# Optimization experiments

Hardware: AMD Instinct MI355X
Metric: run time of the kernel (lower is better)

Reference implementation:

```python
import jax, jax.numpy as jnp
import numpy as np
from jax import lax

B, N, D, H, K = 8, 1024, 384, 6, 7
HD = D // H
EPS = 1e-5


def layer_norm(x, g, b):
    m = jnp.mean(x, axis=-1, keepdims=True)
    v = jnp.mean(jnp.square(x - m), axis=-1, keepdims=True)
    return (x - m) * lax.rsqrt(v + EPS) * g + b


def setup_inputs() -> dict:
    key = jax.random.key(0)
    ks = jax.random.split(key, 12)
    s = 0.02
    return {
        "x": jax.random.normal(ks[0], (B, N, D), jnp.float32),
        "qkv_w": jax.random.normal(ks[1], (3 * D, D), jnp.float32) * s,
        "qkv_b": jnp.zeros((3 * D,), jnp.float32),
        "proj_w": jax.random.normal(ks[2], (D, D), jnp.float32) * s,
        "proj_b": jnp.zeros((D,), jnp.float32),
        "t_before": jnp.eye(H, dtype=jnp.float32) + jax.random.normal(ks[3], (H, H), jnp.float32) * 0.01,
        "t_after": jnp.eye(H, dtype=jnp.float32) + jax.random.normal(ks[4], (H, H), jnp.float32) * 0.01,
        "dw_w": jax.random.normal(ks[5], (D, 1, K), jnp.float32) * s,
        "dw_b": jnp.zeros((D,), jnp.float32),
        "mlp_ln_g": jnp.ones((D,), jnp.float32),
        "mlp_ln_b": jnp.zeros((D,), jnp.float32),
        "norm1_g": jnp.ones((D,), jnp.float32),
        "norm1_b": jnp.zeros((D,), jnp.float32),
        "norm2_g": jnp.ones((D,), jnp.float32),
        "norm2_b": jnp.zeros((D,), jnp.float32),
        "fc1_w": jax.random.normal(ks[6], (4 * D, D), jnp.float32) * s,
        "fc1_b": jnp.zeros((4 * D,), jnp.float32),
        "fc2_w": jax.random.normal(ks[7], (D, 4 * D), jnp.float32) * s,
        "fc2_b": jnp.zeros((D,), jnp.float32),
    }


def reference(x, qkv_w, qkv_b, proj_w, proj_b, t_before, t_after, dw_w, dw_b,
              mlp_ln_g, mlp_ln_b, norm1_g, norm1_b, norm2_g, norm2_b,
              fc1_w, fc1_b, fc2_w, fc2_b):
    # ---- attention branch ----
    h = layer_norm(x, norm1_g, norm1_b)
    qkv = h @ qkv_w.T + qkv_b                                  # (B,N,3D)
    qkv = qkv.reshape(B, N, 3, H, HD).transpose(2, 0, 3, 1, 4)  # (3,B,H,N,hd)
    q, k, v = qkv[0], qkv[1], qkv[2]
    scale = HD ** -0.5
    scores = jnp.einsum('bhnd,bhmd->bhnm', q, k) * scale        # (B,H,N,N)
    scores = jnp.einsum('gh,bhnm->bgnm', t_before, scores)       # head-mix pre-softmax
    probs = jax.nn.softmax(scores, axis=-1)
    probs = jnp.einsum('gh,bhnm->bgnm', t_after, probs)          # head-mix post-softmax
    attn_out = jnp.einsum('bhnm,bhmd->bhnd', probs, v)           # (B,H,N,hd)
    attn_out = attn_out.transpose(0, 2, 1, 3).reshape(B, N, D)
    attn_out = attn_out @ proj_w.T + proj_b
    x = x + attn_out
    # ---- MLP branch ----
    h = layer_norm(x, norm2_g, norm2_b)
    # depthwise conv1d over tokens: (B,D,N), groups=D, same padding
    h_t = h.transpose(0, 2, 1)
    h_t = lax.conv_general_dilated(h_t, dw_w, window_strides=(1,),
                                   padding=[(K // 2, K // 2)],
                                   dimension_numbers=('NCH', 'OIH', 'NCH'),
                                   feature_group_count=D)
    h = h_t.transpose(0, 2, 1) + dw_b
    h = layer_norm(h, mlp_ln_g, mlp_ln_b)
    h = jax.nn.gelu(h @ fc1_w.T + fc1_b, approximate=False)
    h = h @ fc2_w.T + fc2_b
    return x + h
```

## Files before the change

kernel.cpp:

```cpp
#include <hip/hip_runtime.h>
#include <hip/hip_bf16.h>

#define BB 8
#define NN 1024
#define DD 384
#define HH 6
#define HD 64
#define BN 8192
#define D3 1152
#define D4 1536
#define SEC 3145728

typedef __attribute__((ext_vector_type(8))) short short8;
typedef __attribute__((ext_vector_type(4))) float f32x4;

typedef __attribute__((address_space(3))) unsigned char as3_byte;
typedef __attribute__((address_space(1))) const unsigned char as1_byte;

__device__ __forceinline__ void gload16(const void* g, void* l){
  __builtin_amdgcn_global_load_lds((as1_byte*)g, (as3_byte*)l, 16, 0, 0);
}

__device__ __forceinline__ float b2f(unsigned short u){
  union{unsigned int i; float f;} x; x.i=((unsigned int)u)<<16; return x.f;
}
__device__ __forceinline__ unsigned short f2b(float f){
  unsigned int u=__float_as_uint(f);
  return (unsigned short)((u + 0x7FFFu + ((u>>16)&1u))>>16);
}

__global__ void cvt_kernel(const float* __restrict__ w0, const float* __restrict__ w1,
                           const float* __restrict__ w2, const float* __restrict__ w3,
                           unsigned short* __restrict__ out){
  int i = blockIdx.x*256 + threadIdx.x;
  float v;
  if (i < 442368)        v = w0[i];
  else if (i < 589824)   v = w1[i - 442368];
  else if (i < 1179648)  v = w2[i - 589824];
  else if (i < 1769472)  v = w3[i - 1179648];
  else return;
  out[i] = f2b(v);
}

template<int OUTBF>
__global__ __launch_bounds__(128)
void ln_kernel(const float* __restrict__ in, const float* __restrict__ gg, const float* __restrict__ bb,
               float* __restrict__ outf, unsigned short* __restrict__ outb){
  int row = blockIdx.x, t = threadIdx.x;
  const float* r = in + (size_t)row*DD;
  float v0=r[t], v1=r[t+128], v2=r[t+256];
  float s=v0+v1+v2, q=v0*v0+v1*v1+v2*v2;
  #pragma unroll
  for (int o=32;o>0;o>>=1){ s+=__shfl_down(s,o); q+=__shfl_down(q,o); }
  __shared__ float ls[2], lq[2];
  if ((t&63)==0){ ls[t>>6]=s; lq[t>>6]=q; }
  __syncthreads();
  float S=ls[0]+ls[1], Q=lq[0]+lq[1];
  float mean=S*(1.0f/DD);
  float rstd=rsqrtf(Q*(1.0f/DD)-mean*mean+1e-5f);
  float o0=(v0-mean)*rstd*gg[t]+bb[t];
  float o1=(v1-mean)*rstd*gg[t+128]+bb[t+128];
  float o2=(v2-mean)*rstd*gg[t+256]+bb[t+256];
  if (OUTBF){ unsigned short* o=outb+(size_t)row*DD; o[t]=f2b(o0); o[t+128]=f2b(o1); o[t+256]=f2b(o2); }
  else      { float* o=outf+(size_t)row*DD; o[t]=o0; o[t+128]=o1; o[t+256]=o2; }
}

__global__ __launch_bounds__(128)
void conv_ln_kernel(const float* __restrict__ h2, const float* __restrict__ dww, const float* __restrict__ dwb,
                    const float* __restrict__ gg, const float* __restrict__ bb, unsigned short* __restrict__ out){
  int row=blockIdx.x, t=threadIdx.x;
  int bi=row>>10, n=row&1023;
  const float* base = h2 + (size_t)(bi<<10)*DD;
  float a[3];
  #pragma unroll
  for (int j=0;j<3;j++){
    int d=t+j*128;
    float acc=dwb[d];
    #pragma unroll
    for (int k=0;k<7;k++){
      int nn=n+k-3;
      if (nn>=0 && nn<NN) acc += dww[d*7+k]*base[(size_t)nn*DD + d];
    }
    a[j]=acc;
  }
  float s=a[0]+a[1]+a[2], q=a[0]*a[0]+a[1]*a[1]+a[2]*a[2];
  #pragma unroll
  for (int o=32;o>0;o>>=1){ s+=__shfl_down(s,o); q+=__shfl_down(q,o); }
  __shared__ float ls[2], lq[2];
  if ((t&63)==0){ ls[t>>6]=s; lq[t>>6]=q; }
  __syncthreads();
  float S=ls[0]+ls[1], Q=lq[0]+lq[1];
  float mean=S*(1.0f/DD);
  float rstd=rsqrtf(Q*(1.0f/DD)-mean*mean+1e-5f);
  unsigned short* o = out + (size_t)row*DD;
  #pragma unroll
  for (int j=0;j<3;j++){
    int d=t+j*128;
    o[d]=f2b((a[j]-mean)*rstd*gg[d]+bb[d]);
  }
}

template<int MODE, int TN>
__global__ __launch_bounds__(256)
void gemm_kernel(const unsigned short* __restrict__ A, const unsigned short* __restrict__ W,
                 const float* __restrict__ bias, const float* __restrict__ resid,
                 float* __restrict__ outf, unsigned short* __restrict__ outb,
                 int Kdim, int Ncols){
  constexpr int JF = TN/32;
  __shared__ __align__(16) unsigned short lds_a[2][128*32];
  __shared__ __align__(16) unsigned short lds_b[2][TN*32];
  int t=threadIdx.x, lane=t&63, w=t>>6;
  int bm = blockIdx.x*128;
  int bn = blockIdx.y*TN;
  int wr = w>>1, wc = w&1;
  int rm = lane&15, r16 = lane>>4;
  f32x4 acc[4][JF] = {};
  char* ldsa_c = (char*)lds_a;
  char* ldsb_c = (char*)lds_b;
  int abyte[4], bbyte[JF];
  #pragma unroll
  for (int i=0;i<4;i++){
    int ra = wr*64 + i*16 + rm;
    abyte[i] = ra*64 + ((r16 ^ ((ra>>1)&3))*16);
  }
  #pragma unroll
  for (int j=0;j<JF;j++){
    int rb = wc*(TN/2) + j*16 + rm;
    bbyte[j] = rb*64 + ((r16 ^ ((rb>>1)&3))*16);
  }
  auto stage = [&](int buf, int k0){
    #pragma unroll
    for (int c=0;c<2;c++){
      int u = t + c*256;
      int row = u>>2, sl = (u&3) ^ ((row>>1)&3);
      gload16(A + (size_t)(bm+row)*Kdim + k0 + sl*8, ldsa_c + buf*8192 + u*16);
    }
    #pragma unroll
    for (int c=0;c<TN/64;c++){
      int u = t + c*256;
      int row = u>>2, sl = (u&3) ^ ((row>>1)&3);
      gload16(W + (size_t)(bn+row)*Kdim + k0 + sl*8, ldsb_c + buf*(TN*64) + u*16);
    }
  };
  int niter = Kdim>>5;
  stage(0, 0);
  __syncthreads();
  for (int it=0; it<niter; ++it){
    if (it+1<niter) stage((it+1)&1, (it+1)<<5);
    int ab = (it&1)*8192, bb2 = (it&1)*(TN*64);
    short8 af[4], bf[JF];
    #pragma unroll
    for (int i=0;i<4;i++) af[i]=*reinterpret_cast<const short8*>(ldsa_c + ab + abyte[i]);
    #pragma unroll
    for (int j=0;j<JF;j++) bf[j]=*reinterpret_cast<const short8*>(ldsb_c + bb2 + bbyte[j]);
    #pragma unroll
    for (int i=0;i<4;i++)
      #pragma unroll
      for (int j=0;j<JF;j++)
        acc[i][j]=__builtin_amdgcn_mfma_f32_16x16x32_bf16(af[i],bf[j],acc[i][j],0,0,0);
    __syncthreads();
  }
  #pragma unroll
  for (int i=0;i<4;i++){
    #pragma unroll
    for (int j=0;j<JF;j++){
      #pragma unroll
      for (int r=0;r<4;r++){
        int row = bm + wr*64 + i*16 + r16*4 + r;
        int col = bn + wc*(TN/2) + j*16 + rm;
        float v = acc[i][j][r] + bias[col];
        if (MODE==0){
          int c = col/384; int rem = col - c*384; int hh = rem>>6, d = rem&63;
          if (c==0) v *= 0.125f;
          int bi = row>>10, nn = row&1023;
          outb[(size_t)c*SEC + (((size_t)(bi*6+hh))<<16) + (nn<<6) + d] = f2b(v);
        } else if (MODE==1){
          size_t idx = (size_t)row*Ncols + col;
          outf[idx] = resid[idx] + v;
        } else {
          float ge = 0.5f*v*(1.0f+erff(v*0.70710678118654752f));
          outb[(size_t)row*Ncols + col] = f2b(ge);
        }
      }
    }
  }
}

__global__ __launch_bounds__(256)
void vt8_kernel(const unsigned short* __restrict__ V, unsigned char* __restrict__ V8){
  __shared__ unsigned short tile[64][66];
  int z = blockIdx.y, m0 = blockIdx.x*64;
  int t = threadIdx.x, c = t&63, r4 = t>>6;
  #pragma unroll
  for (int p=0;p<16;p++){
    int m = r4 + p*4;
    tile[m][c] = V[((size_t)z<<16) + ((size_t)(m0+m)<<6) + c];
  }
  __syncthreads();
  #pragma unroll
  for (int p=0;p<16;p++){
    int d = r4 + p*4;
    float v = b2f(tile[c][d]);
    int pk = __builtin_amdgcn_cvt_pk_fp8_f32(v, v, 0, false);
    V8[((size_t)z<<16) + ((size_t)d<<10) + m0 + c] = (unsigned char)(pk & 0xff);
  }
}

__global__ __launch_bounds__(512)
void smx_kernel(const unsigned short* __restrict__ qkv,
                const float* __restrict__ tbm, const float* __restrict__ tam,
                unsigned char* __restrict__ P){
  __shared__ __align__(16) unsigned short Qs[6*32*64];
  __shared__ __align__(16) unsigned short Ks[2][6*64*64];
  __shared__ float lred[8][6][16];
  int t=threadIdx.x, lane=t&63, w=t>>6;
  int b = blockIdx.x&7, nt = blockIdx.x>>3;
  int n0 = nt*32;
  int nh = w>>2, mq = (w&3)*16;
  int c16 = lane&15, r16 = lane>>4;
  const unsigned short* kbase = qkv + SEC + (((size_t)(b*6))<<16);
  auto stageK = [&](int buf, int m0){
    #pragma unroll
    for (int i=0;i<6;i++){
      int u = t + i*512;
      int r = u>>3, s = u&7;
      int h = r>>6, m = r&63;
      gload16(kbase + (((size_t)h)<<16) + ((size_t)(m0+m)<<6) + ((s ^ (r&7))*8),
              (char*)Ks + buf*49152 + u*16);
    }
  };
  #pragma unroll
  for (int i=0;i<3;i++){
    int u = t + i*512;
    int r = u>>3, s = u&7;
    int h = r>>5, n = r&31;
    gload16(qkv + (((size_t)(b*6+h))<<16) + ((size_t)(n0+n)<<6) + ((s ^ (r&7))*8),
            (char*)Qs + u*16);
  }
  stageK(0, 0);
  float tbr[36], tar[36];
  #pragma unroll
  for (int i=0;i<36;i++){ tbr[i]=tbm[i]*1.44269504088896f; tar[i]=tam[i]; }
  __syncthreads();
  short8 qf[6][2];
  #pragma unroll
  for (int h=0;h<6;h++){
    int r = h*32 + nh*16 + c16;
    #pragma unroll
    for (int kk=0;kk<2;kk++)
      qf[h][kk] = *(const short8*)((char*)Qs + r*128 + (((kk*4+r16) ^ (r&7))<<4));
  }
  float lsum[6] = {0.f,0.f,0.f,0.f,0.f,0.f};
  float invl[6];
  for (int mt=0; mt<16; ++mt){
    if (mt<15) stageK((mt+1)&1, (mt+1)*64);
    else       stageK(0, 0);
    int kb = (mt&1)*49152;
    f32x4 aq[6] = {};
    #pragma unroll
    for (int h=0;h<6;h++){
      #pragma unroll
      for (int kk=0;kk<2;kk++){
        int r = h*64 + mq + c16;
        short8 kf = *(const short8*)((char*)Ks + kb + r*128 + (((kk*4+r16) ^ (r&7))<<4));
        aq[h] = __builtin_amdgcn_mfma_f32_16x16x32_bf16(kf, qf[h][kk], aq[h], 0,0,0);
      }
    }
    #pragma unroll
    for (int r=0;r<4;r++){
      float s0=aq[0][r], s1=aq[1][r], s2=aq[2][r],
            s3=aq[3][r], s4=aq[4][r], s5=aq[5][r];
      #pragma unroll
      for (int g=0;g<6;g++){
        float sm = tbr[g*6]*s0 + tbr[g*6+1]*s1 + tbr[g*6+2]*s2
                 + tbr[g*6+3]*s3 + tbr[g*6+4]*s4 + tbr[g*6+5]*s5;
        lsum[g] += __builtin_amdgcn_exp2f(sm);
      }
    }
    __syncthreads();
  }
  #pragma unroll
  for (int g=0;g<6;g++){
    lsum[g] += __shfl_xor(lsum[g],16);
    lsum[g] += __shfl_xor(lsum[g],32);
  }
  if (r16==0){
    #pragma unroll
    for (int g=0;g<6;g++) lred[w][g][c16] = lsum[g];
  }
  __syncthreads();
  #pragma unroll
  for (int g=0;g<6;g++)
    invl[g] = 256.0f/(lred[nh*4][g][c16]+lred[nh*4+1][g][c16]
                     +lred[nh*4+2][g][c16]+lred[nh*4+3][g][c16]);
  int nrow = n0 + nh*16 + c16;
  for (int mt=0; mt<16; ++mt){
    int m0 = mt*64;
    if (mt<15) stageK((mt+1)&1, (mt+1)*64);
    int kb = (mt&1)*49152;
    f32x4 aq[6] = {};
    #pragma unroll
    for (int h=0;h<6;h++){
      #pragma unroll
      for (int kk=0;kk<2;kk++){
        int r = h*64 + mq + c16;
        short8 kf = *(const short8*)((char*)Ks + kb + r*128 + (((kk*4+r16) ^ (r&7))<<4));
        aq[h] = __builtin_amdgcn_mfma_f32_16x16x32_bf16(kf, qf[h][kk], aq[h], 0,0,0);
      }
    }
    float pf[6][4];
    #pragma unroll
    for (int r=0;r<4;r++){
      float s0=aq[0][r], s1=aq[1][r], s2=aq[2][r],
            s3=aq[3][r], s4=aq[4][r], s5=aq[5][r];
      float e[6];
      #pragma unroll
      for (int g=0;g<6;g++){
        float sm = tbr[g*6]*s0 + tbr[g*6+1]*s1 + tbr[g*6+2]*s2
                 + tbr[g*6+3]*s3 + tbr[g*6+4]*s4 + tbr[g*6+5]*s5;
        e[g] = __builtin_amdgcn_exp2f(sm) * invl[g];
      }
      #pragma unroll
      for (int g2=0;g2<6;g2++)
        pf[g2][r] = tar[g2*6]*e[0] + tar[g2*6+1]*e[1] + tar[g2*6+2]*e[2]
                  + tar[g2*6+3]*e[3] + tar[g2*6+4]*e[4] + tar[g2*6+5]*e[5];
    }
    #pragma unroll
    for (int g2=0;g2<6;g2++){
      int pkv = __builtin_amdgcn_cvt_pk_fp8_f32(pf[g2][0], pf[g2][1], 0, false);
      pkv = __builtin_amdgcn_cvt_pk_fp8_f32(pf[g2][2], pf[g2][3], pkv, true);
      *(unsigned int*)(P + (((size_t)(b*6+g2))<<20) + ((size_t)nrow<<10) + m0 + mq + r16*4)
        = (unsigned int)pkv;
    }
    __syncthreads();
  }
}

__global__ __launch_bounds__(256)
void pv8_gemm(const unsigned char* __restrict__ P, const unsigned char* __restrict__ V8,
              unsigned short* __restrict__ outp){
  __shared__ __align__(16) unsigned char As[2][64*64];
  __shared__ __align__(16) unsigned char Bs[2][64*64];
  int t=threadIdx.x, lane=t&63, w=t>>6;
  int z = blockIdx.y;
  int bn = blockIdx.x*64;
  int wr = w>>1, wc = w&1;
  int c16=lane&15, r16=lane>>4;
  f32x4 acc[2][2] = {};
  const unsigned char* Pz = P + ((size_t)z<<20);
  const unsigned char* Vz = V8 + ((size_t)z<<16);
  int arow = t>>2, aslot = (t&3) ^ (arow&3);
  auto stage = [&](int buf, int m0){
    gload16(Pz + ((size_t)(bn+arow)<<10) + m0 + aslot*16, (char*)As + buf*4096 + t*16);
    gload16(Vz + ((size_t)arow<<10) + m0 + aslot*16, (char*)Bs + buf*4096 + t*16);
  };
  stage(0, 0);
  __syncthreads();
  for (int mt=0; mt<16; ++mt){
    if (mt+1<16) stage((mt+1)&1, (mt+1)*64);
    int off = (mt&1)*4096;
    #pragma unroll
    for (int kk=0;kk<2;kk++){
      long afr[2], bfr[2];
      #pragma unroll
      for (int i=0;i<2;i++){
        int ra = wr*32 + i*16 + c16;
        int sa = (kk*2 + (r16>>1)) ^ (ra&3);
        afr[i] = *(const long*)((char*)As + off + ra*64 + (sa<<4) + ((r16&1)<<3));
        int rb = wc*32 + i*16 + c16;
        int sb = (kk*2 + (r16>>1)) ^ (rb&3);
        bfr[i] = *(const long*)((char*)Bs + off + rb*64 + (sb<<4) + ((r16&1)<<3));
      }
      #pragma unroll
      for (int i=0;i<2;i++)
        #pragma unroll
        for (int j=0;j<2;j++)
          acc[i][j] = __builtin_amdgcn_mfma_f32_16x16x32_fp8_fp8(afr[i], bfr[j], acc[i][j], 0,0,0);
    }
    __syncthreads();
  }
  int bl = z/6, g = z - bl*6;
  #pragma unroll
  for (int i=0;i<2;i++)
    #pragma unroll
    for (int j=0;j<2;j++)
      #pragma unroll
      for (int r=0;r<4;r++){
        int n = bn + wr*32 + i*16 + r16*4 + r;
        int d = wc*32 + j*16 + c16;
        outp[((size_t)((bl<<10)|n))*DD + g*64 + d] = f2b(acc[i][j][r] * 0.00390625f);
      }
}

extern "C" void kernel_launch(void* const* d_in, const int* in_sizes, int n_in,
                              void* d_out, int out_size, void* d_ws, size_t ws_size,
                              hipStream_t stream){
  const float* x      = (const float*)d_in[0];
  const float* qkv_w  = (const float*)d_in[1];
  const float* qkv_b  = (const float*)d_in[2];
  const float* proj_w = (const float*)d_in[3];
  const float* proj_b = (const float*)d_in[4];
  const float* t_before=(const float*)d_in[5];
  const float* t_after =(const float*)d_in[6];
  const float* dw_w   = (const float*)d_in[7];
  const float* dw_b   = (const float*)d_in[8];
  const float* mlp_g  = (const float*)d_in[9];
  const float* mlp_b  = (const float*)d_in[10];
  const float* n1_g   = (const float*)d_in[11];
  const float* n1_b   = (const float*)d_in[12];
  const float* n2_g   = (const float*)d_in[13];
  const float* n2_b   = (const float*)d_in[14];
  const float* fc1_w  = (const float*)d_in[15];
  const float* fc1_b  = (const float*)d_in[16];
  const float* fc2_w  = (const float*)d_in[17];
  const float* fc2_b  = (const float*)d_in[18];
  float* out = (float*)d_out;
  char* ws = (char*)d_ws;
  unsigned short* qkvwb = (unsigned short*)(ws + 0);
  unsigned short* projwb= (unsigned short*)(ws + 884736);
  unsigned short* fc1wb = (unsigned short*)(ws + 1179648);
  unsigned short* fc2wb = (unsigned short*)(ws + 2359296);
  unsigned short* hb    = (unsigned short*)(ws + 3538944);
  unsigned short* qkvb  = (unsigned short*)(ws + 9830400);
  unsigned char*  V8    = (unsigned char*) (ws + 28704768);
  unsigned char*  Pp    = (unsigned char*) (ws + 34996224);
  unsigned short* attnb = (unsigned short*)(ws + 85327872);
  float*          x2    = (float*)(ws + 91619328);
  float* h2 = (float*)qkvb;
  unsigned short* hcln = hb;
  unsigned short* fc1o = (unsigned short*)Pp;

  cvt_kernel<<<(1769472+255)/256,256,0,stream>>>(qkv_w, proj_w, fc1_w, fc2_w, qkvwb);

  ln_kernel<1><<<BN,128,0,stream>>>(x, n1_g, n1_b, nullptr, hb);
  { dim3 g(BN/128, D3/128); gemm_kernel<0,128><<<g,256,0,stream>>>(hb, qkvwb, qkv_b, nullptr, nullptr, qkvb, DD, D3); }
  { dim3 g(NN/64, 48); vt8_kernel<<<g,256,0,stream>>>(qkvb + 2*(size_t)SEC, V8); }
  smx_kernel<<<256,512,0,stream>>>(qkvb, t_before, t_after, Pp);
  { dim3 g(16, 48); pv8_gemm<<<g,256,0,stream>>>(Pp, V8, attnb); }
  { dim3 g(BN/128, DD/64); gemm_kernel<1,64><<<g,256,0,stream>>>(attnb, projwb, proj_b, x, x2, nullptr, DD, DD); }
  ln_kernel<0><<<BN,128,0,stream>>>(x2, n2_g, n2_b, h2, nullptr);
  conv_ln_kernel<<<BN,128,0,stream>>>(h2, dw_w, dw_b, mlp_g, mlp_b, hcln);
  { dim3 g(BN/128, D4/128); gemm_kernel<2,128><<<g,256,0,stream>>>(hcln, fc1wb, fc1_b, nullptr, nullptr, fc1o, DD, D4); }
  { dim3 g(BN/128, DD/64); gemm_kernel<1,64><<<g,256,0,stream>>>(fc1o, fc2wb, fc2_b, x2, out, nullptr, D4, DD); }
}
```

Before: 211.9 us.

## Single-buffer K tile in softmax kernel to raise occupancy

The K staging buffer in the two-pass softmax kernel shrinks from double to single buffering, roughly halving LDS use, and launch bounds now request 4 blocks per CU. Each iteration reads K fragments into registers, syncs, then issues the next K load so it overlaps the exp and head-mix math. Swizzle address math is hoisted into per-thread precomputed offsets. In exchange the kernel gives up explicit double-buffer prefetch and relies on more resident blocks to hide load latency, and the tighter register budget risks spills.

Result: slower. 247.6 us (+16.8%).

```diff
diff --git a/kernel.cpp b/kernel.cpp
--- a/kernel.cpp
+++ b/kernel.cpp
@@ -206,66 +206,62 @@
   }
 }
 
-__global__ __launch_bounds__(512)
+__global__ __launch_bounds__(512, 4)
 void smx_kernel(const unsigned short* __restrict__ qkv,
                 const float* __restrict__ tbm, const float* __restrict__ tam,
                 unsigned char* __restrict__ P){
   __shared__ __align__(16) unsigned short Qs[6*32*64];
-  __shared__ __align__(16) unsigned short Ks[2][6*64*64];
+  __shared__ __align__(16) unsigned short Ks[6*64*64];
   __shared__ float lred[8][6][16];
   int t=threadIdx.x, lane=t&63, w=t>>6;
   int b = blockIdx.x&7, nt = blockIdx.x>>3;
   int n0 = nt*32;
   int nh = w>>2, mq = (w&3)*16;
   int c16 = lane&15, r16 = lane>>4;
+  int srow = t>>3;
+  int sl = (t&7) ^ (srow&7);
   const unsigned short* kbase = qkv + SEC + (((size_t)(b*6))<<16);
-  auto stageK = [&](int buf, int m0){
-    #pragma unroll
-    for (int i=0;i<6;i++){
-      int u = t + i*512;
-      int r = u>>3, s = u&7;
-      int h = r>>6, m = r&63;
-      gload16(kbase + (((size_t)h)<<16) + ((size_t)(m0+m)<<6) + ((s ^ (r&7))*8),
-              (char*)Ks + buf*49152 + u*16);
-    }
+  #pragma unroll
+  for (int i=0;i<3;i++){
+    int r = srow + i*64;
+    int h = r>>5, n = r&31;
+    gload16(qkv + (((size_t)(b*6+h))<<16) + ((size_t)(n0+n)<<6) + sl*8,
+            (char*)Qs + (t + i*512)*16);
+  }
+  auto stageK = [&](int m0){
+    #pragma unroll
+    for (int i=0;i<6;i++)
+      gload16(kbase + (((size_t)i)<<16) + ((size_t)(m0+srow)<<6) + sl*8,
+              (char*)Ks + (t + i*512)*16);
   };
-  #pragma unroll
-  for (int i=0;i<3;i++){
-    int u = t + i*512;
-    int r = u>>3, s = u&7;
-    int h = r>>5, n = r&31;
-    gload16(qkv + (((size_t)(b*6+h))<<16) + ((size_t)(n0+n)<<6) + ((s ^ (r&7))*8),
-            (char*)Qs + u*16);
-  }
-  stageK(0, 0);
+  stageK(0);
   float tbr[36], tar[36];
   #pragma unroll
   for (int i=0;i<36;i++){ tbr[i]=tbm[i]*1.44269504088896f; tar[i]=tam[i]; }
   __syncthreads();
+  int sw = c16&7;
+  int koff0 = (mq + c16)*128 + ((r16^sw)<<4);
+  int koff1 = (mq + c16)*128 + (((4+r16)^sw)<<4);
   short8 qf[6][2];
   #pragma unroll
   for (int h=0;h<6;h++){
-    int r = h*32 + nh*16 + c16;
-    #pragma unroll
-    for (int kk=0;kk<2;kk++)
-      qf[h][kk] = *(const short8*)((char*)Qs + r*128 + (((kk*4+r16) ^ (r&7))<<4));
+    int qb = (h*32 + nh*16 + c16)*128;
+    qf[h][0] = *(const short8*)((char*)Qs + qb + ((r16^sw)<<4));
+    qf[h][1] = *(const short8*)((char*)Qs + qb + (((4+r16)^sw)<<4));
   }
   float lsum[6] = {0.f,0.f,0.f,0.f,0.f,0.f};
   float invl[6];
   for (int mt=0; mt<16; ++mt){
-    if (mt<15) stageK((mt+1)&1, (mt+1)*64);
-    else       stageK(0, 0);
-    int kb = (mt&1)*49152;
     f32x4 aq[6] = {};
     #pragma unroll
     for (int h=0;h<6;h++){
-      #pragma unroll
-      for (int kk=0;kk<2;kk++){
-        int r = h*64 + mq + c16;
-        short8 kf = *(const short8*)((char*)Ks + kb + r*128 + (((kk*4+r16) ^ (r&7))<<4));
-        aq[h] = __builtin_amdgcn_mfma_f32_16x16x32_bf16(kf, qf[h][kk], aq[h], 0,0,0);
-      }
-    }
+      short8 kf0 = *(const short8*)((char*)Ks + h*8192 + koff0);
+      short8 kf1 = *(const short8*)((char*)Ks + h*8192 + koff1);
+      aq[h] = __builtin_amdgcn_mfma_f32_16x16x32_bf16(kf0, qf[h][0], aq[h], 0,0,0);
+      aq[h] = __builtin_amdgcn_mfma_f32_16x16x32_bf16(kf1, qf[h][1], aq[h], 0,0,0);
+    }
+    __syncthreads();
+    stageK(((mt+1)&15)*64);
     #pragma unroll
     for (int r=0;r<4;r++){
       float s0=aq[0][r], s1=aq[1][r], s2=aq[2][r],
@@ -296,18 +292,16 @@
   int nrow = n0 + nh*16 + c16;
   for (int mt=0; mt<16; ++mt){
     int m0 = mt*64;
-    if (mt<15) stageK((mt+1)&1, (mt+1)*64);
-    int kb = (mt&1)*49152;
     f32x4 aq[6] = {};
     #pragma unroll
     for (int h=0;h<6;h++){
-      #pragma unroll
-      for (int kk=0;kk<2;kk++){
-        int r = h*64 + mq + c16;
-        short8 kf = *(const short8*)((char*)Ks + kb + r*128 + (((kk*4+r16) ^ (r&7))<<4));
-        aq[h] = __builtin_amdgcn_mfma_f32_16x16x32_bf16(kf, qf[h][kk], aq[h], 0,0,0);
-      }
-    }
+      short8 kf0 = *(const short8*)((char*)Ks + h*8192 + koff0);
+      short8 kf1 = *(const short8*)((char*)Ks + h*8192 + koff1);
+      aq[h] = __builtin_amdgcn_mfma_f32_16x16x32_bf16(kf0, qf[h][0], aq[h], 0,0,0);
+      aq[h] = __builtin_amdgcn_mfma_f32_16x16x32_bf16(kf1, qf[h][1], aq[h], 0,0,0);
+    }
+    __syncthreads();
+    if (mt<15) stageK((mt+1)*64);
     float pf[6][4];
     #pragma unroll
     for (int r=0;r<4;r++){
@@ -332,7 +326,7 @@
       *(unsigned int*)(P + (((size_t)(b*6+g2))<<20) + ((size_t)nrow<<10) + m0 + mq + r16*4)
         = (unsigned int)pkv;
     }
-    __syncthreads();
+    if (mt<15) __syncthreads();
   }
 }
 
```
